# Optimization experiments

Measured on AMD Instinct MI355X. Metric: run time of the kernel, lower is better.

The kernel has to match this reference:

```python
import jax, jax.numpy as jnp
import numpy as np

NTYPES = 4
RCUT = 6.0
MIXED_TYPES = False
BOX = 40.0  # Angstrom, sets realistic atomic density


def setup_inputs() -> dict:
    key = jax.random.key(0)
    k1, k2 = jax.random.split(key)
    nframes, nloc = 2, 4096
    coord = jax.random.uniform(k1, (nframes, nloc * 3), dtype=jnp.float32) * BOX
    atype = jax.random.randint(k2, (nframes, nloc), 0, NTYPES, dtype=jnp.int32)
    return {"coord": coord, "atype": atype}


def reference(coord, atype):
    # cell=None branch: extended coords == local coords, nall == nloc
    nframes = coord.shape[0]
    c = coord.reshape(nframes, -1, 3)              # (f, nloc, 3)
    nloc = c.shape[1]
    # diff[f, i, j] = coord[j] - coord[i], shape (f, nloc, nall, 3)
    diff = c[:, None, :, :] - c[:, :, None, :]
    rr2 = jnp.sum(diff * diff, axis=-1)            # (f, nloc, nall)
    # mask self-pairs with inf (torch sets diff rows to inf before squaring)
    eye = jnp.eye(nloc, dtype=bool)
    rr2 = jnp.where(eye[None, :, :], jnp.inf, rr2)
    min_rr2 = jnp.min(rr2, axis=-1)                # (f, nloc)
    mask = rr2 < RCUT ** 2                         # (f, nloc, nall)
    if not MIXED_TYPES:
        # per-type neighbor counts via one-hot contraction (replaces the
        # Python loop over ntypes in the torch code; same math)
        onehot = jax.nn.one_hot(atype, NTYPES, dtype=jnp.int32)  # (f, nall, t)
        nnei = jnp.einsum('fij,fjt->fit', mask.astype(jnp.int32), onehot)
    else:
        valid = (atype >= 0)[:, None, :]
        nnei = jnp.sum(mask & valid, axis=-1).astype(jnp.int32)[..., None]
    max_nnei = jnp.max(nnei, axis=1)               # (f, ntypes) or (f, 1)
    return min_rr2, max_nnei
```

## Files before the change

### kernel.cpp

```cpp
#include <hip/hip_runtime.h>
#include <stdint.h>

#define NFRAMES 2
#define NT 4
#define BLK 256
#define NJ 128

template <bool SELFCHK>
__device__ __forceinline__ void do_pair(float cx, float cy, float cz, unsigned sval,
                                        int j, int i,
                                        float xi, float yi, float zi,
                                        float& mm, unsigned& cc) {
#pragma clang fp contract(off)
    float dx = cx - xi;
    float dy = cy - yi;
    float dz = cz - zi;
    float xx = dx * dx;
    float yy = dy * dy;
    float zz = dz * dz;
    float r2 = (xx + yy) + zz;
    bool self = SELFCHK && (j == i);
    float rm = self ? __builtin_inff() : r2;
    mm = fminf(mm, rm);
    bool near = (r2 < 36.0f) && !self;
    cc += near ? sval : 0u;
}

__global__ __launch_bounds__(BLK) void ns_pair_kernel(const float* __restrict__ coord,
                                                      const int* __restrict__ atype,
                                                      uint2* __restrict__ part,
                                                      int nloc) {
    const int f = blockIdx.z;
    const int half = nloc >> 1;
    const int ibase1 = blockIdx.y * BLK;
    const int ibase2 = ibase1 + half;
    const int i1 = ibase1 + threadIdx.x;
    const int i2 = ibase2 + threadIdx.x;
    const int jslice = nloc / NJ;
    const int jb = blockIdx.x;
    const int jbase = jb * jslice;

    const float* cf = coord + (size_t)f * nloc * 3;
    const int*   tf = atype + (size_t)f * nloc;

    const float x1 = cf[3 * i1], y1 = cf[3 * i1 + 1], z1 = cf[3 * i1 + 2];
    const float x2 = cf[3 * i2], y2 = cf[3 * i2 + 1], z2 = cf[3 * i2 + 2];

    float m1a = __builtin_inff(), m1b = __builtin_inff();
    float m2a = __builtin_inff(), m2b = __builtin_inff();
    unsigned c1a = 0u, c1b = 0u, c2a = 0u, c2b = 0u;

    const bool overlap = (jbase >= ibase1 && jbase < ibase1 + BLK) ||
                         (jbase >= ibase2 && jbase < ibase2 + BLK);

    if (overlap) {
#pragma unroll 4
        for (int j = jbase; j < jbase + jslice; j += 2) {
            float cx0 = cf[3 * j],     cy0 = cf[3 * j + 1], cz0 = cf[3 * j + 2];
            unsigned s0 = 1u << (tf[j] * 8);
            do_pair<true>(cx0, cy0, cz0, s0, j, i1, x1, y1, z1, m1a, c1a);
            do_pair<true>(cx0, cy0, cz0, s0, j, i2, x2, y2, z2, m2a, c2a);
            float cx1 = cf[3 * j + 3], cy1 = cf[3 * j + 4], cz1 = cf[3 * j + 5];
            unsigned s1 = 1u << (tf[j + 1] * 8);
            do_pair<true>(cx1, cy1, cz1, s1, j + 1, i1, x1, y1, z1, m1b, c1b);
            do_pair<true>(cx1, cy1, cz1, s1, j + 1, i2, x2, y2, z2, m2b, c2b);
        }
    } else {
#pragma unroll 4
        for (int j = jbase; j < jbase + jslice; j += 2) {
            float cx0 = cf[3 * j],     cy0 = cf[3 * j + 1], cz0 = cf[3 * j + 2];
            unsigned s0 = 1u << (tf[j] * 8);
            do_pair<false>(cx0, cy0, cz0, s0, j, i1, x1, y1, z1, m1a, c1a);
            do_pair<false>(cx0, cy0, cz0, s0, j, i2, x2, y2, z2, m2a, c2a);
            float cx1 = cf[3 * j + 3], cy1 = cf[3 * j + 4], cz1 = cf[3 * j + 5];
            unsigned s1 = 1u << (tf[j + 1] * 8);
            do_pair<false>(cx1, cy1, cz1, s1, j + 1, i1, x1, y1, z1, m1b, c1b);
            do_pair<false>(cx1, cy1, cz1, s1, j + 1, i2, x2, y2, z2, m2b, c2b);
        }
    }

    const size_t base = ((size_t)jb * NFRAMES + f) * nloc;
    part[base + i1] = make_uint2(__float_as_uint(fminf(m1a, m1b)), c1a + c1b);
    part[base + i2] = make_uint2(__float_as_uint(fminf(m2a, m2b)), c2a + c2b);
}

__global__ __launch_bounds__(BLK) void ns_finalize_kernel(const uint2* __restrict__ part,
                                                          float* __restrict__ out,
                                                          int* __restrict__ pmax,
                                                          int nloc) {
    const int nbpf = nloc / BLK;
    const int f  = blockIdx.x / nbpf;
    const int ib = blockIdx.x % nbpf;
    const int i  = ib * BLK + threadIdx.x;

    float ma = __builtin_inff(), mb = __builtin_inff();
    unsigned ca = 0u, cb = 0u;
#pragma unroll 8
    for (int jb = 0; jb < NJ; jb += 2) {
        uint2 va = part[((size_t)jb * NFRAMES + f) * nloc + i];
        uint2 vb = part[((size_t)(jb + 1) * NFRAMES + f) * nloc + i];
        ma = fminf(ma, __uint_as_float(va.x));
        mb = fminf(mb, __uint_as_float(vb.x));
        ca += va.y;
        cb += vb.y;
    }
    out[(size_t)f * nloc + i] = fminf(ma, mb);
    unsigned c = ca + cb;

    int m0 = (int)(c & 255u);
    int m1 = (int)((c >> 8) & 255u);
    int m2 = (int)((c >> 16) & 255u);
    int m3 = (int)(c >> 24);
    for (int off = 32; off > 0; off >>= 1) {
        m0 = max(m0, __shfl_xor(m0, off, 64));
        m1 = max(m1, __shfl_xor(m1, off, 64));
        m2 = max(m2, __shfl_xor(m2, off, 64));
        m3 = max(m3, __shfl_xor(m3, off, 64));
    }
    __shared__ int red[BLK / 64][NT];
    int wid = threadIdx.x >> 6;
    if ((threadIdx.x & 63) == 0) {
        red[wid][0] = m0; red[wid][1] = m1; red[wid][2] = m2; red[wid][3] = m3;
    }
    __syncthreads();
    if (threadIdx.x < NT) {
        int t = threadIdx.x;
        pmax[blockIdx.x * NT + t] =
            max(max(red[0][t], red[1][t]), max(red[2][t], red[3][t]));
    }
}

__global__ __launch_bounds__(64) void ns_max_kernel(const int* __restrict__ pmax,
                                                    float* __restrict__ out,
                                                    int nbpf, int nloc) {
    const int t = threadIdx.x;
    if (t < NFRAMES * NT) {
        const int f = t / NT, tt = t % NT;
        int m = 0;
        for (int b = 0; b < nbpf; ++b)
            m = max(m, pmax[(f * nbpf + b) * NT + tt]);
        out[(size_t)NFRAMES * nloc + f * NT + tt] = (float)m;
    }
}

extern "C" void kernel_launch(void* const* d_in, const int* in_sizes, int n_in,
                              void* d_out, int out_size, void* d_ws, size_t ws_size,
                              hipStream_t stream) {
    const float* coord = (const float*)d_in[0];
    const int*   atype = (const int*)d_in[1];
    const int nloc = in_sizes[1] / NFRAMES;

    float* out = (float*)d_out;
    uint2* part = (uint2*)d_ws;
    int*   pmax = (int*)((char*)d_ws + (size_t)NJ * NFRAMES * nloc * sizeof(uint2));

    dim3 grid(NJ, nloc / (BLK * 2), NFRAMES);
    ns_pair_kernel<<<grid, dim3(BLK), 0, stream>>>(coord, atype, part, nloc);

    const int nbpf = nloc / BLK;
    ns_finalize_kernel<<<NFRAMES * nbpf, BLK, 0, stream>>>(part, out, pmax, nloc);

    ns_max_kernel<<<1, 64, 0, stream>>>(pmax, out, nbpf, nloc);
}
```

Before: 27.28 us.

## Raise i-atoms per thread to four and fold max reduction into atomics

The pair kernel now gives each thread four i-atoms instead of two, so every loaded j coordinate feeds more pair evaluations and the pair grid is half as large. The third kernel is removed: the finalize blocks (now 128 threads) write per-type maxima with atomicMax on float bits, and the pair kernel zeroes those output slots first. This trades more registers per thread and fewer blocks (lower occupancy) for less load traffic and one fewer launch. The zeroing relies on the pair kernel finishing before finalize on the same stream.

Measured after the change: 26.52 us. 2.8% less time.

```diff
diff --git a/kernel.cpp b/kernel.cpp
--- a/kernel.cpp
+++ b/kernel.cpp
@@ -5,6 +5,8 @@
 #define NT 4
 #define BLK 256
 #define NJ 128
+#define IPT 4
+#define FBLK 128
 
 template <bool SELFCHK>
 __device__ __forceinline__ void do_pair(float cx, float cy, float cz, unsigned sval,
@@ -20,92 +22,103 @@
     float zz = dz * dz;
     float r2 = (xx + yy) + zz;
     bool self = SELFCHK && (j == i);
-    float rm = self ? __builtin_inff() : r2;
-    mm = fminf(mm, rm);
+    mm = fminf(mm, self ? __builtin_inff() : r2);
     bool near = (r2 < 36.0f) && !self;
     cc += near ? sval : 0u;
+}
+
+template <bool SELFCHK>
+__device__ __forceinline__ void pair_body(const float* __restrict__ cf,
+                                          const int* __restrict__ tf,
+                                          int jbase, int jslice,
+                                          const int (&ii)[IPT],
+                                          const float (&xi)[IPT],
+                                          const float (&yi)[IPT],
+                                          const float (&zi)[IPT],
+                                          float (&ma)[IPT], float (&mb)[IPT],
+                                          unsigned (&ca)[IPT], unsigned (&cb)[IPT]) {
+#pragma unroll 4
+    for (int j = jbase; j < jbase + jslice; j += 2) {
+        float cx0 = cf[3 * j], cy0 = cf[3 * j + 1], cz0 = cf[3 * j + 2];
+        unsigned s0 = 1u << (tf[j] * 8);
+#pragma unroll
+        for (int k = 0; k < IPT; ++k)
+            do_pair<SELFCHK>(cx0, cy0, cz0, s0, j, ii[k], xi[k], yi[k], zi[k], ma[k], ca[k]);
+        float cx1 = cf[3 * j + 3], cy1 = cf[3 * j + 4], cz1 = cf[3 * j + 5];
+        unsigned s1 = 1u << (tf[j + 1] * 8);
+#pragma unroll
+        for (int k = 0; k < IPT; ++k)
+            do_pair<SELFCHK>(cx1, cy1, cz1, s1, j + 1, ii[k], xi[k], yi[k], zi[k], mb[k], cb[k]);
+    }
 }
 
 __global__ __launch_bounds__(BLK) void ns_pair_kernel(const float* __restrict__ coord,
                                                       const int* __restrict__ atype,
                                                       uint2* __restrict__ part,
+                                                      float* __restrict__ out,
                                                       int nloc) {
     const int f = blockIdx.z;
-    const int half = nloc >> 1;
-    const int ibase1 = blockIdx.y * BLK;
-    const int ibase2 = ibase1 + half;
-    const int i1 = ibase1 + threadIdx.x;
-    const int i2 = ibase2 + threadIdx.x;
+    const int q = nloc >> 2;
+    const int ib = blockIdx.y * BLK;
     const int jslice = nloc / NJ;
     const int jb = blockIdx.x;
     const int jbase = jb * jslice;
 
+    if (blockIdx.x == 0 && blockIdx.y == 0 && blockIdx.z == 0 &&
+        threadIdx.x < NFRAMES * NT)
+        ((unsigned*)out)[(size_t)NFRAMES * nloc + threadIdx.x] = 0u;
+
     const float* cf = coord + (size_t)f * nloc * 3;
     const int*   tf = atype + (size_t)f * nloc;
 
-    const float x1 = cf[3 * i1], y1 = cf[3 * i1 + 1], z1 = cf[3 * i1 + 2];
-    const float x2 = cf[3 * i2], y2 = cf[3 * i2 + 1], z2 = cf[3 * i2 + 2];
-
-    float m1a = __builtin_inff(), m1b = __builtin_inff();
-    float m2a = __builtin_inff(), m2b = __builtin_inff();
-    unsigned c1a = 0u, c1b = 0u, c2a = 0u, c2b = 0u;
-
-    const bool overlap = (jbase >= ibase1 && jbase < ibase1 + BLK) ||
-                         (jbase >= ibase2 && jbase < ibase2 + BLK);
-
-    if (overlap) {
-#pragma unroll 4
-        for (int j = jbase; j < jbase + jslice; j += 2) {
-            float cx0 = cf[3 * j],     cy0 = cf[3 * j + 1], cz0 = cf[3 * j + 2];
-            unsigned s0 = 1u << (tf[j] * 8);
-            do_pair<true>(cx0, cy0, cz0, s0, j, i1, x1, y1, z1, m1a, c1a);
-            do_pair<true>(cx0, cy0, cz0, s0, j, i2, x2, y2, z2, m2a, c2a);
-            float cx1 = cf[3 * j + 3], cy1 = cf[3 * j + 4], cz1 = cf[3 * j + 5];
-            unsigned s1 = 1u << (tf[j + 1] * 8);
-            do_pair<true>(cx1, cy1, cz1, s1, j + 1, i1, x1, y1, z1, m1b, c1b);
-            do_pair<true>(cx1, cy1, cz1, s1, j + 1, i2, x2, y2, z2, m2b, c2b);
-        }
-    } else {
-#pragma unroll 4
-        for (int j = jbase; j < jbase + jslice; j += 2) {
-            float cx0 = cf[3 * j],     cy0 = cf[3 * j + 1], cz0 = cf[3 * j + 2];
-            unsigned s0 = 1u << (tf[j] * 8);
-            do_pair<false>(cx0, cy0, cz0, s0, j, i1, x1, y1, z1, m1a, c1a);
-            do_pair<false>(cx0, cy0, cz0, s0, j, i2, x2, y2, z2, m2a, c2a);
-            float cx1 = cf[3 * j + 3], cy1 = cf[3 * j + 4], cz1 = cf[3 * j + 5];
-            unsigned s1 = 1u << (tf[j + 1] * 8);
-            do_pair<false>(cx1, cy1, cz1, s1, j + 1, i1, x1, y1, z1, m1b, c1b);
-            do_pair<false>(cx1, cy1, cz1, s1, j + 1, i2, x2, y2, z2, m2b, c2b);
-        }
+    int ii[IPT];
+    float xi[IPT], yi[IPT], zi[IPT];
+    float ma[IPT], mb[IPT];
+    unsigned ca[IPT], cb[IPT];
+    bool ov = false;
+#pragma unroll
+    for (int k = 0; k < IPT; ++k) {
+        const int base = ib + k * q;
+        ii[k] = base + threadIdx.x;
+        xi[k] = cf[3 * ii[k]];
+        yi[k] = cf[3 * ii[k] + 1];
+        zi[k] = cf[3 * ii[k] + 2];
+        ma[k] = mb[k] = __builtin_inff();
+        ca[k] = cb[k] = 0u;
+        ov |= (jbase >= base) && (jbase < base + BLK);
     }
 
-    const size_t base = ((size_t)jb * NFRAMES + f) * nloc;
-    part[base + i1] = make_uint2(__float_as_uint(fminf(m1a, m1b)), c1a + c1b);
-    part[base + i2] = make_uint2(__float_as_uint(fminf(m2a, m2b)), c2a + c2b);
+    if (ov)
+        pair_body<true >(cf, tf, jbase, jslice, ii, xi, yi, zi, ma, mb, ca, cb);
+    else
+        pair_body<false>(cf, tf, jbase, jslice, ii, xi, yi, zi, ma, mb, ca, cb);
+
+    const size_t pb = ((size_t)jb * NFRAMES + f) * nloc;
+#pragma unroll
+    for (int k = 0; k < IPT; ++k)
+        part[pb + ii[k]] = make_uint2(__float_as_uint(fminf(ma[k], mb[k])), ca[k] + cb[k]);
 }
 
-__global__ __launch_bounds__(BLK) void ns_finalize_kernel(const uint2* __restrict__ part,
-                                                          float* __restrict__ out,
-                                                          int* __restrict__ pmax,
-                                                          int nloc) {
-    const int nbpf = nloc / BLK;
-    const int f  = blockIdx.x / nbpf;
-    const int ib = blockIdx.x % nbpf;
-    const int i  = ib * BLK + threadIdx.x;
+__global__ __launch_bounds__(FBLK) void ns_finalize_kernel(const uint2* __restrict__ part,
+                                                           float* __restrict__ out,
+                                                           int nloc) {
+    const int nbpf = nloc / FBLK;
+    const int f = blockIdx.x / nbpf;
+    const int i = (blockIdx.x % nbpf) * FBLK + threadIdx.x;
 
     float ma = __builtin_inff(), mb = __builtin_inff();
-    unsigned ca = 0u, cb = 0u;
+    unsigned cacc = 0u, cbacc = 0u;
 #pragma unroll 8
     for (int jb = 0; jb < NJ; jb += 2) {
         uint2 va = part[((size_t)jb * NFRAMES + f) * nloc + i];
         uint2 vb = part[((size_t)(jb + 1) * NFRAMES + f) * nloc + i];
         ma = fminf(ma, __uint_as_float(va.x));
         mb = fminf(mb, __uint_as_float(vb.x));
-        ca += va.y;
-        cb += vb.y;
+        cacc += va.y;
+        cbacc += vb.y;
     }
     out[(size_t)f * nloc + i] = fminf(ma, mb);
-    unsigned c = ca + cb;
+    const unsigned c = cacc + cbacc;
 
     int m0 = (int)(c & 255u);
     int m1 = (int)((c >> 8) & 255u);
@@ -117,29 +130,17 @@
         m2 = max(m2, __shfl_xor(m2, off, 64));
         m3 = max(m3, __shfl_xor(m3, off, 64));
     }
-    __shared__ int red[BLK / 64][NT];
-    int wid = threadIdx.x >> 6;
+    __shared__ int red[FBLK / 64][NT];
+    const int wid = threadIdx.x >> 6;
     if ((threadIdx.x & 63) == 0) {
         red[wid][0] = m0; red[wid][1] = m1; red[wid][2] = m2; red[wid][3] = m3;
     }
     __syncthreads();
     if (threadIdx.x < NT) {
-        int t = threadIdx.x;
-        pmax[blockIdx.x * NT + t] =
-            max(max(red[0][t], red[1][t]), max(red[2][t], red[3][t]));
-    }
-}
-
-__global__ __launch_bounds__(64) void ns_max_kernel(const int* __restrict__ pmax,
-                                                    float* __restrict__ out,
-                                                    int nbpf, int nloc) {
-    const int t = threadIdx.x;
-    if (t < NFRAMES * NT) {
-        const int f = t / NT, tt = t % NT;
-        int m = 0;
-        for (int b = 0; b < nbpf; ++b)
-            m = max(m, pmax[(f * nbpf + b) * NT + tt]);
-        out[(size_t)NFRAMES * nloc + f * NT + tt] = (float)m;
+        const int t = threadIdx.x;
+        const int m = max(red[0][t], red[1][t]);
+        atomicMax((unsigned*)out + (size_t)NFRAMES * nloc + f * NT + t,
+                  __float_as_uint((float)m));
     }
 }
 
@@ -150,15 +151,12 @@
     const int*   atype = (const int*)d_in[1];
     const int nloc = in_sizes[1] / NFRAMES;
 
-    float* out = (float*)d_out;
+    float* out  = (float*)d_out;
     uint2* part = (uint2*)d_ws;
-    int*   pmax = (int*)((char*)d_ws + (size_t)NJ * NFRAMES * nloc * sizeof(uint2));
 
-    dim3 grid(NJ, nloc / (BLK * 2), NFRAMES);
-    ns_pair_kernel<<<grid, dim3(BLK), 0, stream>>>(coord, atype, part, nloc);
+    dim3 grid(NJ, nloc / (BLK * IPT), NFRAMES);
+    ns_pair_kernel<<<grid, dim3(BLK), 0, stream>>>(coord, atype, part, out, nloc);
 
-    const int nbpf = nloc / BLK;
-    ns_finalize_kernel<<<NFRAMES * nbpf, BLK, 0, stream>>>(part, out, pmax, nloc);
-
-    ns_max_kernel<<<1, 64, 0, stream>>>(pmax, out, nbpf, nloc);
+    const int nbpf = nloc / FBLK;
+    ns_finalize_kernel<<<NFRAMES * nbpf, FBLK, 0, stream>>>(part, out, nloc);
 }
```
